# Kernel optimization log

Hardware: AMD Instinct MI355X
Metric: run time of the kernel (lower is better)

Reference implementation:

```python
import jax, jax.numpy as jnp
import numpy as np

N, L, S, E, D = 8, 2048, 2048, 1024, 64

def setup_inputs() -> dict:
    key = jax.random.key(0)
    ks = jax.random.split(key, 6)
    q = jax.random.normal(ks[0], (N, L, E), dtype=jnp.float32)
    k = jax.random.normal(ks[1], (N, S, E), dtype=jnp.float32)
    v = jax.random.normal(ks[2], (N, S, E), dtype=jnp.float32)
    # Linear weights stored as [E, D] so projection is x @ W
    Wq = jax.random.normal(ks[3], (E, D), dtype=jnp.float32) / np.sqrt(E)
    Wk = jax.random.normal(ks[4], (E, D), dtype=jnp.float32) / np.sqrt(E)
    Wv = jax.random.normal(ks[5], (E, D), dtype=jnp.float32) / np.sqrt(E)
    # causal bool mask: True above diagonal => masked to -inf
    attn_mask = jnp.triu(jnp.ones((L, S), dtype=bool), k=1)
    return {"q": q, "k": k, "v": v, "Wq": Wq, "Wk": Wk, "Wv": Wv, "attn_mask": attn_mask}


def reference(q, k, v, Wq, Wk, Wv, attn_mask):
    qh = q @ Wq                      # [N, L, D]
    kh = k @ Wk                      # [N, S, D]
    vh = v @ Wv                      # [N, S, D]
    # NOTE: source divides by d**(-1/2), i.e. multiplies by sqrt(D) (faithful bug)
    scale = jnp.asarray(D, dtype=qh.dtype) ** 0.5
    scores = jnp.einsum("nld,nsd->nls", qh, kh) * scale   # [N, L, S]
    scores = jnp.where(attn_mask[None, :, :], -jnp.inf, scores)
    weights = jax.nn.softmax(scores, axis=-1)
    out = jnp.einsum("nls,nsd->nld", weights, vh)          # [N, L, D]
    return out
```

## Files before the change

kernel.cpp:

```cpp
#include <hip/hip_runtime.h>
#include <math.h>

#define NB 8
#define LQ 2048
#define EE 1024
#define DD 64
#define MROWS (NB * LQ)

typedef __attribute__((ext_vector_type(4))) float f32x4;
typedef __attribute__((ext_vector_type(8))) short s16x8;
typedef __attribute__((ext_vector_type(4))) short s16x4;
typedef __attribute__((ext_vector_type(4))) int i32x4;

__device__ __forceinline__ unsigned f2bf_u(float f) {
  unsigned u = __builtin_bit_cast(unsigned, f);
  u += 0x7FFFu + ((u >> 16) & 1u);
  return u >> 16;
}
__device__ __forceinline__ float bf2f(unsigned h) {
  unsigned u = h << 16;
  return __builtin_bit_cast(float, u);
}

__global__ __launch_bounds__(256) void wsplit_kernel(
    const float* __restrict__ Wq, const float* __restrict__ Wk,
    const float* __restrict__ Wv, short* __restrict__ wt) {
  int bk = blockIdx.x;
  int z = blockIdx.y;
  const float* W = (z == 0) ? Wq : (z == 1) ? Wk : Wv;
  __shared__ float tile[64][65];
  int t = threadIdx.x;
#pragma unroll
  for (int it = 0; it < 16; ++it) {
    int kk = it * 4 + (t >> 6);
    int d = t & 63;
    tile[kk][d] = W[(size_t)(bk * 64 + kk) * 64 + d];
  }
  __syncthreads();
#pragma unroll
  for (int it = 0; it < 16; ++it) {
    int d = it * 4 + (t >> 6);
    int kk = t & 63;
    float f = tile[kk][d];
    unsigned h = f2bf_u(f);
    unsigned l = f2bf_u(f - bf2f(h));
    wt[((size_t)(z * 2 + 0) * 64 + d) * 1024 + bk * 64 + kk] = (short)h;
    wt[((size_t)(z * 2 + 1) * 64 + d) * 1024 + bk * 64 + kk] = (short)l;
  }
}

__global__ __launch_bounds__(256, 2) void proj_kernel(
    const float* __restrict__ xq, const float* __restrict__ xk,
    const float* __restrict__ xv, const short* __restrict__ wt,
    int* __restrict__ qkp, short* __restrict__ vhp) {
  int z = blockIdx.y;
  const float* x = (z == 0) ? xq : (z == 1) ? xk : xv;
  const short* wthi = wt + (size_t)(z * 2 + 0) * 64 * 1024;
  const short* wtlo = wt + (size_t)(z * 2 + 1) * 64 * 1024;
  int row0 = blockIdx.x * 128;
  __shared__ short xs_hi[128][72];
  __shared__ short xs_lo[128][72];
  __shared__ short wh[64][72];
  __shared__ short wl[64][72];
  int t = threadIdx.x;
  int wv = t >> 6, lane = t & 63;
  int c = lane & 15, quad = lane >> 4;
  f32x4 acc[2][4] = {};
  for (int kb = 0; kb < 16; ++kb) {
#pragma unroll
    for (int it = 0; it < 8; ++it) {
      int flat4 = it * 256 + t;
      int r = flat4 >> 4, c4 = (flat4 & 15) * 4;
      f32x4 xv4 = *(const f32x4*)&x[(size_t)(row0 + r) * 1024 + kb * 64 + c4];
      s16x4 h, l;
#pragma unroll
      for (int j = 0; j < 4; ++j) {
        unsigned hh = f2bf_u(xv4[j]);
        h[j] = (short)hh;
        l[j] = (short)f2bf_u(xv4[j] - bf2f(hh));
      }
      *(s16x4*)&xs_hi[r][c4] = h;
      *(s16x4*)&xs_lo[r][c4] = l;
    }
#pragma unroll
    for (int it = 0; it < 4; ++it) {
      int flat4 = it * 256 + t;
      int d = flat4 >> 4, k4 = (flat4 & 15) * 4;
      *(s16x4*)&wh[d][k4] = *(const s16x4*)&wthi[(size_t)d * 1024 + kb * 64 + k4];
      *(s16x4*)&wl[d][k4] = *(const s16x4*)&wtlo[(size_t)d * 1024 + kb * 64 + k4];
    }
    __syncthreads();
#pragma unroll
    for (int kc = 0; kc < 2; ++kc) {
      s16x8 ah[2], al[2], bh[4], bl[4];
#pragma unroll
      for (int rs = 0; rs < 2; ++rs) {
        ah[rs] = *(const s16x8*)&xs_hi[wv * 32 + rs * 16 + c][kc * 32 + quad * 8];
        al[rs] = *(const s16x8*)&xs_lo[wv * 32 + rs * 16 + c][kc * 32 + quad * 8];
      }
#pragma unroll
      for (int cs = 0; cs < 4; ++cs) {
        bh[cs] = *(const s16x8*)&wh[cs * 16 + c][kc * 32 + quad * 8];
        bl[cs] = *(const s16x8*)&wl[cs * 16 + c][kc * 32 + quad * 8];
      }
#pragma unroll
      for (int rs = 0; rs < 2; ++rs)
#pragma unroll
        for (int cs = 0; cs < 4; ++cs) {
          acc[rs][cs] = __builtin_amdgcn_mfma_f32_16x16x32_bf16(ah[rs], bh[cs], acc[rs][cs], 0, 0, 0);
          acc[rs][cs] = __builtin_amdgcn_mfma_f32_16x16x32_bf16(ah[rs], bl[cs], acc[rs][cs], 0, 0, 0);
          acc[rs][cs] = __builtin_amdgcn_mfma_f32_16x16x32_bf16(al[rs], bh[cs], acc[rs][cs], 0, 0, 0);
        }
    }
    __syncthreads();
  }
#pragma unroll
  for (int rs = 0; rs < 2; ++rs)
#pragma unroll
    for (int cs = 0; cs < 4; ++cs)
#pragma unroll
      for (int r = 0; r < 4; ++r) {
        int row = row0 + wv * 32 + rs * 16 + quad * 4 + r;
        int col = cs * 16 + c;
        float val = acc[rs][cs][r];
        if (z < 2) {
          unsigned h = f2bf_u(val);
          unsigned l = f2bf_u(val - bf2f(h));
          qkp[(size_t)z * MROWS * 64 + (size_t)row * 64 + col] = (int)(h | (l << 16));
        } else {
          vhp[(size_t)row * 64 + col] = (short)f2bf_u(val);
        }
      }
}

__global__ __launch_bounds__(256) void attn_kernel(
    const int* __restrict__ qkp, const short* __restrict__ vhp,
    float* __restrict__ outp) {
  int qt = blockIdx.x;
  int n = blockIdx.y;
  const int* qp = qkp;
  const int* kp = qkp + (size_t)MROWS * 64;
  __shared__ short ksh[64][72];
  __shared__ short ksl[64][72];
  __shared__ short vT[64][68];
  __shared__ short pS[4][16][72];
  int t = threadIdx.x;
  int wv = t >> 6, lane = t & 63;
  int c = lane & 15, quad = lane >> 4;
  int qr0 = qt * 64;
  s16x8 qfh[2], qfl[2];
  size_t qbase = ((size_t)n * LQ + qr0 + wv * 16 + c) * 64;
#pragma unroll
  for (int kc = 0; kc < 2; ++kc) {
    i32x4 v0 = *(const i32x4*)&qp[qbase + kc * 32 + quad * 8];
    i32x4 v1 = *(const i32x4*)&qp[qbase + kc * 32 + quad * 8 + 4];
#pragma unroll
    for (int j = 0; j < 4; ++j) {
      qfh[kc][j] = (short)(v0[j] & 0xffff);
      qfl[kc][j] = (short)(((unsigned)v0[j]) >> 16);
      qfh[kc][4 + j] = (short)(v1[j] & 0xffff);
      qfl[kc][4 + j] = (short)(((unsigned)v1[j]) >> 16);
    }
  }
  f32x4 o[4] = {};
  float m_r[4], l_r[4];
#pragma unroll
  for (int r = 0; r < 4; ++r) { m_r[r] = -INFINITY; l_r[r] = 0.0f; }

  for (int kt = 0; kt <= qt; ++kt) {
    int s0 = kt * 64;
#pragma unroll
    for (int it = 0; it < 4; ++it) {
      int idx = it * 256 + t;
      int s = idx >> 4, d4 = (idx & 15) * 4;
      size_t g = ((size_t)n * LQ + s0 + s) * 64 + d4;
      i32x4 kv = *(const i32x4*)&kp[g];
      s16x4 h, l;
#pragma unroll
      for (int j = 0; j < 4; ++j) {
        h[j] = (short)(kv[j] & 0xffff);
        l[j] = (short)(((unsigned)kv[j]) >> 16);
      }
      *(s16x4*)&ksh[s][d4] = h;
      *(s16x4*)&ksl[s][d4] = l;
      s16x4 vv = *(const s16x4*)&vhp[g];
#pragma unroll
      for (int j = 0; j < 4; ++j) vT[d4 + j][s] = vv[j];
    }
    __syncthreads();
    f32x4 sa[4] = {};
#pragma unroll
    for (int ct = 0; ct < 4; ++ct) {
#pragma unroll
      for (int kc = 0; kc < 2; ++kc) {
        s16x8 bh = *(const s16x8*)&ksh[ct * 16 + c][kc * 32 + quad * 8];
        s16x8 bl = *(const s16x8*)&ksl[ct * 16 + c][kc * 32 + quad * 8];
        sa[ct] = __builtin_amdgcn_mfma_f32_16x16x32_bf16(qfh[kc], bh, sa[ct], 0, 0, 0);
        sa[ct] = __builtin_amdgcn_mfma_f32_16x16x32_bf16(qfh[kc], bl, sa[ct], 0, 0, 0);
        sa[ct] = __builtin_amdgcn_mfma_f32_16x16x32_bf16(qfl[kc], bh, sa[ct], 0, 0, 0);
      }
    }
    float sv[4][4];
    bool diag = (kt == qt);
#pragma unroll
    for (int ct = 0; ct < 4; ++ct)
#pragma unroll
      for (int r = 0; r < 4; ++r) {
        float xsc = sa[ct][r] * 8.0f;
        if (diag) {
          int sg = s0 + ct * 16 + c;
          int qg = qr0 + wv * 16 + quad * 4 + r;
          if (sg > qg) xsc = -INFINITY;
        }
        sv[ct][r] = xsc;
      }
    float alpha[4];
#pragma unroll
    for (int r = 0; r < 4; ++r) {
      float mx = fmaxf(fmaxf(sv[0][r], sv[1][r]), fmaxf(sv[2][r], sv[3][r]));
#pragma unroll
      for (int off = 1; off < 16; off <<= 1) mx = fmaxf(mx, __shfl_xor(mx, off, 64));
      float mnew = fmaxf(m_r[r], mx);
      alpha[r] = exp2f((m_r[r] - mnew) * 1.44269504088896f);
      m_r[r] = mnew;
      float rs = 0.0f;
#pragma unroll
      for (int ct = 0; ct < 4; ++ct) {
        float p = exp2f((sv[ct][r] - mnew) * 1.44269504088896f);
        sv[ct][r] = p;
        rs += p;
      }
#pragma unroll
      for (int off = 1; off < 16; off <<= 1) rs += __shfl_xor(rs, off, 64);
      l_r[r] = l_r[r] * alpha[r] + rs;
    }
#pragma unroll
    for (int dt = 0; dt < 4; ++dt)
#pragma unroll
      for (int r = 0; r < 4; ++r) o[dt][r] *= alpha[r];
#pragma unroll
    for (int ct = 0; ct < 4; ++ct)
#pragma unroll
      for (int r = 0; r < 4; ++r)
        pS[wv][quad * 4 + r][ct * 16 + c] = (short)f2bf_u(sv[ct][r]);
    s16x8 pa[2];
#pragma unroll
    for (int kc2 = 0; kc2 < 2; ++kc2)
      pa[kc2] = *(const s16x8*)&pS[wv][c][kc2 * 32 + quad * 8];
#pragma unroll
    for (int dt = 0; dt < 4; ++dt) {
#pragma unroll
      for (int kc2 = 0; kc2 < 2; ++kc2) {
        s16x4 v0 = *(const s16x4*)&vT[dt * 16 + c][kc2 * 32 + quad * 8];
        s16x4 v1 = *(const s16x4*)&vT[dt * 16 + c][kc2 * 32 + quad * 8 + 4];
        s16x8 vb;
#pragma unroll
        for (int j = 0; j < 4; ++j) { vb[j] = v0[j]; vb[4 + j] = v1[j]; }
        o[dt] = __builtin_amdgcn_mfma_f32_16x16x32_bf16(pa[kc2], vb, o[dt], 0, 0, 0);
      }
    }
    __syncthreads();
  }
#pragma unroll
  for (int dt = 0; dt < 4; ++dt)
#pragma unroll
    for (int r = 0; r < 4; ++r) {
      int row = qr0 + wv * 16 + quad * 4 + r;
      outp[((size_t)n * LQ + row) * 64 + dt * 16 + c] = o[dt][r] / l_r[r];
    }
}

extern "C" void kernel_launch(void* const* d_in, const int* in_sizes, int n_in,
                              void* d_out, int out_size, void* d_ws, size_t ws_size,
                              hipStream_t stream) {
  const float* q = (const float*)d_in[0];
  const float* k = (const float*)d_in[1];
  const float* v = (const float*)d_in[2];
  const float* Wq = (const float*)d_in[3];
  const float* Wk = (const float*)d_in[4];
  const float* Wv = (const float*)d_in[5];
  float* out = (float*)d_out;

  char* ws = (char*)d_ws;
  short* wt = (short*)ws;
  int* qkp = (int*)(ws + 786432);
  short* vhp = (short*)(ws + 786432 + 8388608);

  wsplit_kernel<<<dim3(16, 3), 256, 0, stream>>>(Wq, Wk, Wv, wt);
  proj_kernel<<<dim3(128, 3), 256, 0, stream>>>(q, k, v, wt, qkp, vhp);
  attn_kernel<<<dim3(32, 8), 256, 0, stream>>>(qkp, vhp, out);
}
```

Measured before the change: 300.9 us.

## Drop LDS staging, split hi/lo planes, transpose V, use single-wave attention blocks

The projection kernel now feeds MFMA operands straight from global memory instead of staging x and W tiles through shared memory. Q/K are written as separate hi and lo bf16 planes, and V is written pre-transposed through a shared-memory tile. Attention moves from 256-thread blocks over 64 query rows to 64-thread single-wave blocks over 16 rows (1024 blocks). Each wave reads K and V fragments directly from global or L2 with no block barriers. This gives finer causal load balance and more parallel blocks, at the cost of losing shared K/V reuse across waves and doing uncoalesced global reads.

```diff
diff --git a/kernel.cpp b/kernel.cpp
--- a/kernel.cpp
+++ b/kernel.cpp
@@ -3,14 +3,9 @@
 
 #define NB 8
 #define LQ 2048
-#define EE 1024
-#define DD 64
-#define MROWS (NB * LQ)
 
 typedef __attribute__((ext_vector_type(4))) float f32x4;
 typedef __attribute__((ext_vector_type(8))) short s16x8;
-typedef __attribute__((ext_vector_type(4))) short s16x4;
-typedef __attribute__((ext_vector_type(4))) int i32x4;
 
 __device__ __forceinline__ unsigned f2bf_u(float f) {
   unsigned u = __builtin_bit_cast(unsigned, f);
@@ -21,6 +16,8 @@
   unsigned u = h << 16;
   return __builtin_bit_cast(float, u);
 }
+
+#define MFMA16 __builtin_amdgcn_mfma_f32_16x16x32_bf16
 
 __global__ __launch_bounds__(256) void wsplit_kernel(
     const float* __restrict__ Wq, const float* __restrict__ Wk,
@@ -49,159 +46,144 @@
   }
 }
 
-__global__ __launch_bounds__(256, 2) void proj_kernel(
+__global__ __launch_bounds__(256) void proj_kernel(
     const float* __restrict__ xq, const float* __restrict__ xk,
     const float* __restrict__ xv, const short* __restrict__ wt,
-    int* __restrict__ qkp, short* __restrict__ vhp) {
+    short* __restrict__ qhi, short* __restrict__ qlo,
+    short* __restrict__ khi, short* __restrict__ klo,
+    short* __restrict__ vhT) {
   int z = blockIdx.y;
   const float* x = (z == 0) ? xq : (z == 1) ? xk : xv;
   const short* wthi = wt + (size_t)(z * 2 + 0) * 64 * 1024;
   const short* wtlo = wt + (size_t)(z * 2 + 1) * 64 * 1024;
   int row0 = blockIdx.x * 128;
-  __shared__ short xs_hi[128][72];
-  __shared__ short xs_lo[128][72];
-  __shared__ short wh[64][72];
-  __shared__ short wl[64][72];
   int t = threadIdx.x;
   int wv = t >> 6, lane = t & 63;
   int c = lane & 15, quad = lane >> 4;
   f32x4 acc[2][4] = {};
+  const float* xr0 = x + (size_t)(row0 + wv * 32 + c) * 1024;
+  const float* xr1 = xr0 + 16 * 1024;
   for (int kb = 0; kb < 16; ++kb) {
 #pragma unroll
-    for (int it = 0; it < 8; ++it) {
-      int flat4 = it * 256 + t;
-      int r = flat4 >> 4, c4 = (flat4 & 15) * 4;
-      f32x4 xv4 = *(const f32x4*)&x[(size_t)(row0 + r) * 1024 + kb * 64 + c4];
-      s16x4 h, l;
-#pragma unroll
-      for (int j = 0; j < 4; ++j) {
-        unsigned hh = f2bf_u(xv4[j]);
-        h[j] = (short)hh;
-        l[j] = (short)f2bf_u(xv4[j] - bf2f(hh));
-      }
-      *(s16x4*)&xs_hi[r][c4] = h;
-      *(s16x4*)&xs_lo[r][c4] = l;
-    }
-#pragma unroll
-    for (int it = 0; it < 4; ++it) {
-      int flat4 = it * 256 + t;
-      int d = flat4 >> 4, k4 = (flat4 & 15) * 4;
-      *(s16x4*)&wh[d][k4] = *(const s16x4*)&wthi[(size_t)d * 1024 + kb * 64 + k4];
-      *(s16x4*)&wl[d][k4] = *(const s16x4*)&wtlo[(size_t)d * 1024 + kb * 64 + k4];
-    }
-    __syncthreads();
-#pragma unroll
     for (int kc = 0; kc < 2; ++kc) {
-      s16x8 ah[2], al[2], bh[4], bl[4];
+      int ko = kb * 64 + kc * 32 + quad * 8;
+      s16x8 ah[2], al[2];
 #pragma unroll
       for (int rs = 0; rs < 2; ++rs) {
-        ah[rs] = *(const s16x8*)&xs_hi[wv * 32 + rs * 16 + c][kc * 32 + quad * 8];
-        al[rs] = *(const s16x8*)&xs_lo[wv * 32 + rs * 16 + c][kc * 32 + quad * 8];
+        const float* xr = rs ? xr1 : xr0;
+        f32x4 a0 = *(const f32x4*)&xr[ko];
+        f32x4 a1 = *(const f32x4*)&xr[ko + 4];
+#pragma unroll
+        for (int j = 0; j < 4; ++j) {
+          unsigned h0 = f2bf_u(a0[j]);
+          ah[rs][j] = (short)h0;
+          al[rs][j] = (short)f2bf_u(a0[j] - bf2f(h0));
+          unsigned h1 = f2bf_u(a1[j]);
+          ah[rs][4 + j] = (short)h1;
+          al[rs][4 + j] = (short)f2bf_u(a1[j] - bf2f(h1));
+        }
       }
 #pragma unroll
       for (int cs = 0; cs < 4; ++cs) {
-        bh[cs] = *(const s16x8*)&wh[cs * 16 + c][kc * 32 + quad * 8];
-        bl[cs] = *(const s16x8*)&wl[cs * 16 + c][kc * 32 + quad * 8];
-      }
-#pragma unroll
-      for (int rs = 0; rs < 2; ++rs)
-#pragma unroll
-        for (int cs = 0; cs < 4; ++cs) {
-          acc[rs][cs] = __builtin_amdgcn_mfma_f32_16x16x32_bf16(ah[rs], bh[cs], acc[rs][cs], 0, 0, 0);
-          acc[rs][cs] = __builtin_amdgcn_mfma_f32_16x16x32_bf16(ah[rs], bl[cs], acc[rs][cs], 0, 0, 0);
-          acc[rs][cs] = __builtin_amdgcn_mfma_f32_16x16x32_bf16(al[rs], bh[cs], acc[rs][cs], 0, 0, 0);
-        }
-    }
-    __syncthreads();
-  }
-#pragma unroll
-  for (int rs = 0; rs < 2; ++rs)
-#pragma unroll
-    for (int cs = 0; cs < 4; ++cs)
-#pragma unroll
-      for (int r = 0; r < 4; ++r) {
-        int row = row0 + wv * 32 + rs * 16 + quad * 4 + r;
-        int col = cs * 16 + c;
-        float val = acc[rs][cs][r];
-        if (z < 2) {
+        s16x8 bh = *(const s16x8*)&wthi[(size_t)(cs * 16 + c) * 1024 + ko];
+        s16x8 bl = *(const s16x8*)&wtlo[(size_t)(cs * 16 + c) * 1024 + ko];
+#pragma unroll
+        for (int rs = 0; rs < 2; ++rs) {
+          acc[rs][cs] = MFMA16(ah[rs], bh, acc[rs][cs], 0, 0, 0);
+          acc[rs][cs] = MFMA16(ah[rs], bl, acc[rs][cs], 0, 0, 0);
+          acc[rs][cs] = MFMA16(al[rs], bh, acc[rs][cs], 0, 0, 0);
+        }
+      }
+    }
+  }
+  if (z < 2) {
+    short* hi = (z == 0) ? qhi : khi;
+    short* lo = (z == 0) ? qlo : klo;
+#pragma unroll
+    for (int rs = 0; rs < 2; ++rs)
+#pragma unroll
+      for (int cs = 0; cs < 4; ++cs)
+#pragma unroll
+        for (int r = 0; r < 4; ++r) {
+          int row = row0 + wv * 32 + rs * 16 + quad * 4 + r;
+          int col = cs * 16 + c;
+          float val = acc[rs][cs][r];
           unsigned h = f2bf_u(val);
           unsigned l = f2bf_u(val - bf2f(h));
-          qkp[(size_t)z * MROWS * 64 + (size_t)row * 64 + col] = (int)(h | (l << 16));
-        } else {
-          vhp[(size_t)row * 64 + col] = (short)f2bf_u(val);
-        }
-      }
-}
-
-__global__ __launch_bounds__(256) void attn_kernel(
-    const int* __restrict__ qkp, const short* __restrict__ vhp,
-    float* __restrict__ outp) {
-  int qt = blockIdx.x;
-  int n = blockIdx.y;
-  const int* qp = qkp;
-  const int* kp = qkp + (size_t)MROWS * 64;
-  __shared__ short ksh[64][72];
-  __shared__ short ksl[64][72];
-  __shared__ short vT[64][68];
-  __shared__ short pS[4][16][72];
-  int t = threadIdx.x;
-  int wv = t >> 6, lane = t & 63;
+          hi[(size_t)row * 64 + col] = (short)h;
+          lo[(size_t)row * 64 + col] = (short)l;
+        }
+  } else {
+    __shared__ short vtile[64][136];
+#pragma unroll
+    for (int rs = 0; rs < 2; ++rs)
+#pragma unroll
+      for (int cs = 0; cs < 4; ++cs)
+#pragma unroll
+        for (int r = 0; r < 4; ++r) {
+          int rl = wv * 32 + rs * 16 + quad * 4 + r;
+          vtile[cs * 16 + c][rl] = (short)f2bf_u(acc[rs][cs][r]);
+        }
+    __syncthreads();
+    int n = row0 >> 11;
+    int sbase = row0 & 2047;
+    int d = t >> 2, sc = (t & 3) * 32;
+#pragma unroll
+    for (int j = 0; j < 4; ++j) {
+      s16x8 vv = *(const s16x8*)&vtile[d][sc + j * 8];
+      *(s16x8*)&vhT[((size_t)n * 64 + d) * LQ + sbase + sc + j * 8] = vv;
+    }
+  }
+}
+
+__global__ __launch_bounds__(64) void attn_kernel(
+    const short* __restrict__ qhi, const short* __restrict__ qlo,
+    const short* __restrict__ khi, const short* __restrict__ klo,
+    const short* __restrict__ vhT, float* __restrict__ outp) {
+  int bid = blockIdx.x;
+  int n = bid & 7;
+  int qt = bid >> 3;
+  int lane = threadIdx.x;
   int c = lane & 15, quad = lane >> 4;
-  int qr0 = qt * 64;
+  int qr0 = qt * 16;
+  __shared__ short pS[16][72];
   s16x8 qfh[2], qfl[2];
-  size_t qbase = ((size_t)n * LQ + qr0 + wv * 16 + c) * 64;
+  size_t qbase = ((size_t)n * LQ + qr0 + c) * 64;
 #pragma unroll
   for (int kc = 0; kc < 2; ++kc) {
-    i32x4 v0 = *(const i32x4*)&qp[qbase + kc * 32 + quad * 8];
-    i32x4 v1 = *(const i32x4*)&qp[qbase + kc * 32 + quad * 8 + 4];
-#pragma unroll
-    for (int j = 0; j < 4; ++j) {
-      qfh[kc][j] = (short)(v0[j] & 0xffff);
-      qfl[kc][j] = (short)(((unsigned)v0[j]) >> 16);
-      qfh[kc][4 + j] = (short)(v1[j] & 0xffff);
-      qfl[kc][4 + j] = (short)(((unsigned)v1[j]) >> 16);
-    }
+    qfh[kc] = *(const s16x8*)&qhi[qbase + kc * 32 + quad * 8];
+    qfl[kc] = *(const s16x8*)&qlo[qbase + kc * 32 + quad * 8];
   }
   f32x4 o[4] = {};
   float m_r[4], l_r[4];
 #pragma unroll
   for (int r = 0; r < 4; ++r) { m_r[r] = -INFINITY; l_r[r] = 0.0f; }
-
-  for (int kt = 0; kt <= qt; ++kt) {
+  int ktmax = qt >> 2;
+  for (int kt = 0; kt <= ktmax; ++kt) {
     int s0 = kt * 64;
-#pragma unroll
-    for (int it = 0; it < 4; ++it) {
-      int idx = it * 256 + t;
-      int s = idx >> 4, d4 = (idx & 15) * 4;
-      size_t g = ((size_t)n * LQ + s0 + s) * 64 + d4;
-      i32x4 kv = *(const i32x4*)&kp[g];
-      s16x4 h, l;
-#pragma unroll
-      for (int j = 0; j < 4; ++j) {
-        h[j] = (short)(kv[j] & 0xffff);
-        l[j] = (short)(((unsigned)kv[j]) >> 16);
-      }
-      *(s16x4*)&ksh[s][d4] = h;
-      *(s16x4*)&ksl[s][d4] = l;
-      s16x4 vv = *(const s16x4*)&vhp[g];
-#pragma unroll
-      for (int j = 0; j < 4; ++j) vT[d4 + j][s] = vv[j];
-    }
-    __syncthreads();
+    size_t kbase = ((size_t)n * LQ + s0) * 64;
     f32x4 sa[4] = {};
 #pragma unroll
     for (int ct = 0; ct < 4; ++ct) {
+      size_t rb = kbase + (size_t)(ct * 16 + c) * 64;
 #pragma unroll
       for (int kc = 0; kc < 2; ++kc) {
-        s16x8 bh = *(const s16x8*)&ksh[ct * 16 + c][kc * 32 + quad * 8];
-        s16x8 bl = *(const s16x8*)&ksl[ct * 16 + c][kc * 32 + quad * 8];
-        sa[ct] = __builtin_amdgcn_mfma_f32_16x16x32_bf16(qfh[kc], bh, sa[ct], 0, 0, 0);
-        sa[ct] = __builtin_amdgcn_mfma_f32_16x16x32_bf16(qfh[kc], bl, sa[ct], 0, 0, 0);
-        sa[ct] = __builtin_amdgcn_mfma_f32_16x16x32_bf16(qfl[kc], bh, sa[ct], 0, 0, 0);
-      }
-    }
+        s16x8 bh = *(const s16x8*)&khi[rb + kc * 32 + quad * 8];
+        s16x8 bl = *(const s16x8*)&klo[rb + kc * 32 + quad * 8];
+        sa[ct] = MFMA16(qfh[kc], bh, sa[ct], 0, 0, 0);
+        sa[ct] = MFMA16(qfh[kc], bl, sa[ct], 0, 0, 0);
+        sa[ct] = MFMA16(qfl[kc], bh, sa[ct], 0, 0, 0);
+      }
+    }
+    s16x8 vb[4][2];
+#pragma unroll
+    for (int dt = 0; dt < 4; ++dt)
+#pragma unroll
+      for (int kc2 = 0; kc2 < 2; ++kc2)
+        vb[dt][kc2] = *(const s16x8*)&vhT[((size_t)n * 64 + dt * 16 + c) * LQ +
+                                          s0 + kc2 * 32 + quad * 8];
     float sv[4][4];
-    bool diag = (kt == qt);
+    bool diag = (kt == ktmax);
 #pragma unroll
     for (int ct = 0; ct < 4; ++ct)
 #pragma unroll
@@ -209,7 +191,7 @@
         float xsc = sa[ct][r] * 8.0f;
         if (diag) {
           int sg = s0 + ct * 16 + c;
-          int qg = qr0 + wv * 16 + quad * 4 + r;
+          int qg = qr0 + quad * 4 + r;
           if (sg > qg) xsc = -INFINITY;
         }
         sv[ct][r] = xsc;
@@ -242,32 +224,23 @@
     for (int ct = 0; ct < 4; ++ct)
 #pragma unroll
       for (int r = 0; r < 4; ++r)
-        pS[wv][quad * 4 + r][ct * 16 + c] = (short)f2bf_u(sv[ct][r]);
+        pS[quad * 4 + r][ct * 16 + c] = (short)f2bf_u(sv[ct][r]);
     s16x8 pa[2];
 #pragma unroll
     for (int kc2 = 0; kc2 < 2; ++kc2)
-      pa[kc2] = *(const s16x8*)&pS[wv][c][kc2 * 32 + quad * 8];
-#pragma unroll
-    for (int dt = 0; dt < 4; ++dt) {
-#pragma unroll
-      for (int kc2 = 0; kc2 < 2; ++kc2) {
-        s16x4 v0 = *(const s16x4*)&vT[dt * 16 + c][kc2 * 32 + quad * 8];
-        s16x4 v1 = *(const s16x4*)&vT[dt * 16 + c][kc2 * 32 + quad * 8 + 4];
-        s16x8 vb;
-#pragma unroll
-        for (int j = 0; j < 4; ++j) { vb[j] = v0[j]; vb[4 + j] = v1[j]; }
-        o[dt] = __builtin_amdgcn_mfma_f32_16x16x32_bf16(pa[kc2], vb, o[dt], 0, 0, 0);
-      }
-    }
-    __syncthreads();
+      pa[kc2] = *(const s16x8*)&pS[c][kc2 * 32 + quad * 8];
+#pragma unroll
+    for (int dt = 0; dt < 4; ++dt)
+#pragma unroll
+      for (int kc2 = 0; kc2 < 2; ++kc2)
+        o[dt] = MFMA16(pa[kc2], vb[dt][kc2], o[dt], 0, 0, 0);
   }
 #pragma unroll
   for (int dt = 0; dt < 4; ++dt)
 #pragma unroll
-    for (int r = 0; r < 4; ++r) {
-      int row = qr0 + wv * 16 + quad * 4 + r;
-      outp[((size_t)n * LQ + row) * 64 + dt * 16 + c] = o[dt][r] / l_r[r];
-    }
+    for (int r = 0; r < 4; ++r)
+      outp[((size_t)n * LQ + qr0 + quad * 4 + r) * 64 + dt * 16 + c] =
+          o[dt][r] / l_r[r];
 }
 
 extern "C" void kernel_launch(void* const* d_in, const int* in_sizes, int n_in,
@@ -282,11 +255,14 @@
   float* out = (float*)d_out;
 
   char* ws = (char*)d_ws;
-  short* wt = (short*)ws;
-  int* qkp = (int*)(ws + 786432);
-  short* vhp = (short*)(ws + 786432 + 8388608);
+  short* wt  = (short*)ws;
+  short* qhi = (short*)(ws + 786432);
+  short* qlo = qhi + (size_t)16384 * 64;
+  short* khi = qlo + (size_t)16384 * 64;
+  short* klo = khi + (size_t)16384 * 64;
+  short* vhT = klo + (size_t)16384 * 64;
 
   wsplit_kernel<<<dim3(16, 3), 256, 0, stream>>>(Wq, Wk, Wv, wt);
-  proj_kernel<<<dim3(128, 3), 256, 0, stream>>>(q, k, v, wt, qkp, vhp);
-  attn_kernel<<<dim3(32, 8), 256, 0, stream>>>(qkp, vhp, out);
-}
+  proj_kernel<<<dim3(128, 3), 256, 0, stream>>>(q, k, v, wt, qhi, qlo, khi, klo, vhT);
+  attn_kernel<<<dim3(1024), 64, 0, stream>>>(qhi, qlo, khi, klo, vhT, out);
+}
```

New measurement: 341.3 us. +13.4%, slower.
